# Kernel tuning notes

Hardware: AMD Instinct MI355X
Metric: run time of the kernel (lower is better)

Reference implementation:

```python
import jax, jax.numpy as jnp
import numpy as np

N_QUBITS = 10
N_LAYERS = 2

# ---- batched statevector simulator helpers (state shape: (B,) + (2,)*n) ----

def _apply1q(state, w, mat):
    # mat: [2,2] complex, same for all batch elements
    s = jnp.moveaxis(state, w + 1, 1)
    s = jnp.einsum('ij,bj...->bi...', mat, s)
    return jnp.moveaxis(s, 1, w + 1)

def _apply1q_b(state, w, mats):
    # mats: [B,2,2] complex, per-batch gate (input-encoding RY)
    s = jnp.moveaxis(state, w + 1, 1)
    s = jnp.einsum('bij,bj...->bi...', mats, s)
    return jnp.moveaxis(s, 1, w + 1)

def _cnot(state, c, t):
    s = jnp.moveaxis(state, (c + 1, t + 1), (1, 2))  # [B,2(ctrl),2(tgt),...]
    s = jnp.concatenate([s[:, :1], jnp.flip(s[:, 1:2], axis=2)], axis=1)
    return jnp.moveaxis(s, (1, 2), (c + 1, t + 1))

def _rz(t):
    p = jnp.exp(-0.5j * t.astype(jnp.complex64))
    z = jnp.zeros((), jnp.complex64)
    return jnp.stack([jnp.stack([p, z]), jnp.stack([z, jnp.conj(p)])])

def _rx(t):
    h = 0.5 * t
    c = jnp.cos(h).astype(jnp.complex64)
    s = jnp.sin(h).astype(jnp.complex64) * (-1j)
    return jnp.stack([jnp.stack([c, s]), jnp.stack([s, c])])

def _ry(t):
    h = 0.5 * t
    c, s = jnp.cos(h), jnp.sin(h)
    return jnp.stack([jnp.stack([c, -s]), jnp.stack([s, c])]).astype(jnp.complex64)

def qlayer(angles, qparams):
    """angles: [B, n_qubits] float -> [B, n_qubits] PauliZ expectations."""
    B = angles.shape[0]
    n = N_QUBITS
    state = jnp.zeros((B,) + (2,) * n, jnp.complex64)
    state = state.at[(slice(None),) + (0,) * n].set(1.0)
    # data-encoding RY with per-batch angles
    half = 0.5 * angles
    c, s = jnp.cos(half), jnp.sin(half)
    for w in range(n):
        row0 = jnp.stack([c[:, w], -s[:, w]], -1)
        row1 = jnp.stack([s[:, w], c[:, w]], -1)
        mats = jnp.stack([row0, row1], 1).astype(jnp.complex64)  # [B,2,2]
        state = _apply1q_b(state, w, mats)
    for l in range(N_LAYERS):
        for w in range(n):
            state = _apply1q(state, w, _rz(qparams[l, w, 0]))
            state = _apply1q(state, w, _rx(qparams[l, w, 1]))
            state = _apply1q(state, w, _ry(qparams[l, w, 2]))
        for w in range(n - 1):
            state = _cnot(state, w, w + 1)
        state = _cnot(state, n - 1, 0)
    probs = jnp.real(state * jnp.conj(state))
    exps = []
    for w in range(n):
        axes = tuple(a for a in range(1, n + 1) if a != w + 1)
        p = jnp.sum(probs, axis=axes)  # [B,2]
        exps.append(p[:, 0] - p[:, 1])
    return jnp.stack(exps, -1)


def setup_inputs() -> dict:
    key = jax.random.key(0)
    ks = jax.random.split(key, 12)
    T, B, D, H = 64, 256, 32, N_QUBITS
    in_dim = D + H
    std = 1.0 / np.sqrt(in_dim)
    inputs = jax.random.normal(ks[0], (T, B, D), jnp.float32)
    qparams = 0.01 * jax.random.normal(ks[1], (N_LAYERS, N_QUBITS, 3), jnp.float32)
    def lin(k1, k2):
        W = jax.random.uniform(k1, (H, in_dim), jnp.float32, -std, std)
        b = jax.random.uniform(k2, (H,), jnp.float32, -std, std)
        return W, b
    W_f, b_f = lin(ks[2], ks[3])
    W_i, b_i = lin(ks[4], ks[5])
    W_g, b_g = lin(ks[6], ks[7])
    W_o, b_o = lin(ks[8], ks[9])
    return dict(inputs=inputs, qparams=qparams, W_f=W_f, b_f=b_f, W_i=W_i, b_i=b_i,
                W_g=W_g, b_g=b_g, W_o=W_o, b_o=b_o)


def reference(inputs, qparams, W_f, b_f, W_i, b_i, W_g, b_g, W_o, b_o):
    T, B, D = inputs.shape
    H = N_QUBITS

    def step(carry, x):
        hx, cx = carry
        comb = jnp.concatenate([x, hx], axis=1)  # [B, D+H]
        pre = jnp.concatenate([
            comb @ W_f.T + b_f,
            comb @ W_i.T + b_i,
            comb @ W_g.T + b_g,
            comb @ W_o.T + b_o,
        ], axis=0)  # [4B, H] -- one fused circuit call for all 4 gates
        q = qlayer(pre, qparams).reshape(4, B, H)
        f = jax.nn.sigmoid(q[0])
        i = jax.nn.sigmoid(q[1])
        g = jnp.tanh(q[2])
        o = jax.nn.sigmoid(q[3])
        cx2 = f * cx + i * g
        hx2 = o * jnp.tanh(cx2)
        return (hx2, cx2), hx2

    hx = jnp.zeros((B, H), jnp.float32)
    cx = jnp.zeros((B, H), jnp.float32)
    (hx, cx), outputs = jax.lax.scan(jax.checkpoint(step), (hx, cx), inputs)
    return outputs, hx, cx
```

## Files before the change

kernel.cpp:

```cpp
#include <hip/hip_runtime.h>

#define TS 64
#define NB 256
#define DI 32
#define NH 10
#define IND 42

template<int CTRL>
__device__ __forceinline__ float dppx(float v){
  return __int_as_float(__builtin_amdgcn_update_dpp(
      0, __float_as_int(v), CTRL, 0xF, 0xF, true));
}

__device__ __forceinline__ float rl(float v, int lane){
  return __int_as_float(__builtin_amdgcn_readlane(__float_as_int(v), lane));
}

__device__ __forceinline__ void pin(float& x){ asm volatile("" : "+v"(x)); }

__device__ __forceinline__ float sigm(float x){ return 1.f/(1.f + __expf(-x)); }
__device__ __forceinline__ float tanhr(float x){ float e = __expf(2.f*x); return 1.f - 2.f/(e + 1.f); }

__device__ __forceinline__ void mkU(float t1, float t2, float t3, float* dst){
  float c1 = __cosf(0.5f*t1), s1 = __sinf(0.5f*t1);
  float c2 = __cosf(0.5f*t2), s2 = __sinf(0.5f*t2);
  float c3 = __cosf(0.5f*t3), s3 = __sinf(0.5f*t3);
  float A00r =  c2*c1, A00i = -c2*s1;
  float A01r =  s2*s1, A01i = -s2*c1;
  float A10r = -s2*s1, A10i = -s2*c1;
  float A11r =  c2*c1, A11i =  c2*s1;
  dst[0] = c3*A00r - s3*A10r; dst[1] = c3*A00i - s3*A10i;
  dst[2] = c3*A01r - s3*A11r; dst[3] = c3*A01i - s3*A11i;
  dst[4] = s3*A00r + c3*A10r; dst[5] = s3*A00i + c3*A10i;
  dst[6] = s3*A01r + c3*A11r; dst[7] = s3*A01i + c3*A11i;
}

__device__ __forceinline__ float3 qf(float q00, float q11, float q01){
  return make_float3(0.5f*(q00+q11), 0.5f*(q00-q11), 0.5f*q01);
}
__device__ __forceinline__ float qeval(float3 q, float C, float S){
  return fmaf(q.y, C, fmaf(q.z, S, q.x));
}

__global__ __launch_bounds__(256) __attribute__((amdgpu_waves_per_eu(1, 1)))
void qlstm_kernel(const float* __restrict__ xin,
                  const float* __restrict__ qp,
                  const float* __restrict__ Wf, const float* __restrict__ bfp,
                  const float* __restrict__ Wi, const float* __restrict__ bip,
                  const float* __restrict__ Wg, const float* __restrict__ bgp,
                  const float* __restrict__ Wo, const float* __restrict__ bop,
                  float* __restrict__ out)
{
  __shared__ float lx[TS][DI + 1];
  __shared__ float lwx[4][TS][NH];
  __shared__ __align__(16) float lBw[4][NH][4];
  __shared__ __align__(16) float lq[2][NH][4];

  const int tid  = threadIdx.x;
  const int b    = blockIdx.x;
  const int g    = tid >> 6;
  const int lane = tid & 63;
  const int hq   = lane >> 2;
  const int sg   = lane & 3;
  const int hrow = (lane < NH) ? lane : 0;

  const float* Wsel = (g==0) ? Wf : (g==1) ? Wi : (g==2) ? Wg : Wo;
  const float* bsel = (g==0) ? bfp : (g==1) ? bip : (g==2) ? bgp : bop;

  for (int i = tid; i < TS*DI; i += 256) {
    int tt = i >> 5, d = i & 31;
    lx[tt][d] = xin[(size_t)tt*(NB*DI) + b*DI + d];
  }
  if (lane < NH) {
    float u[8];
    mkU(qp[30 + lane*3 + 0], qp[30 + lane*3 + 1], qp[30 + lane*3 + 2], u);
    float B00 = u[0]*u[0]+u[1]*u[1] - (u[4]*u[4]+u[5]*u[5]);
    float B11 = u[2]*u[2]+u[3]*u[3] - (u[6]*u[6]+u[7]*u[7]);
    float B01r= u[0]*u[2]+u[1]*u[3] - (u[4]*u[6]+u[5]*u[7]);
    float B01i= u[1]*u[2]-u[0]*u[3] - (u[5]*u[6]-u[4]*u[7]);
    *reinterpret_cast<float4*>(&lBw[g][lane][0]) = make_float4(B00,B11,B01r,B01i);
  }
  __syncthreads();

  {
    float acc[NH];
    #pragma unroll
    for (int h = 0; h < NH; h++) acc[h] = bsel[h];
    for (int k = 0; k < DI; k++) {
      float xk = lx[lane][k];
      #pragma unroll
      for (int h = 0; h < NH; h++) acc[h] = fmaf(Wsel[h*IND + k], xk, acc[h]);
    }
    #pragma unroll
    for (int h = 0; h < NH; h++) lwx[g][lane][h] = acc[h];
  }

  float wh[NH];
  #pragma unroll
  for (int j = 0; j < NH; j++) wh[j] = Wsel[hrow*IND + DI + j];

  float3 Qn0, Qn1, Qer, Qei;
  {
    float U1[8];
    mkU(qp[hrow*3+0], qp[hrow*3+1], qp[hrow*3+2], U1);
    float r00r=U1[0], r00i=U1[1], r01r=U1[2], r01i=U1[3];
    float r10r=U1[4], r10i=U1[5], r11r=U1[6], r11i=U1[7];
    float P0r,P0i,P1r,P1i, R0r,R0i,R1r,R1i;
    if (lane == 0) {
      P0r=r00r; P0i=r00i; P1r=r01r; P1i=r01i;
      R0r=r10r; R0i=r10i; R1r=r11r; R1i=r11i;
    } else {
      P0r=0.5f*(r00r+r10r); P0i=0.5f*(r00i+r10i);
      P1r=0.5f*(r01r+r11r); P1i=0.5f*(r01i+r11i);
      R0r=0.5f*(r00r-r10r); R0i=0.5f*(r00i-r10i);
      R1r=0.5f*(r01r-r11r); R1i=0.5f*(r01i-r11i);
    }
    Qn0 = qf(P0r*P0r+P0i*P0i, P1r*P1r+P1i*P1i, 2.f*(P0r*P1r+P0i*P1i));
    Qn1 = qf(R0r*R0r+R0i*R0i, R1r*R1r+R1i*R1i, 2.f*(R0r*R1r+R0i*R1i));
    Qer = qf(R0r*P0r+R0i*P0i, R1r*P1r+R1i*P1i,
             (R0r*P1r+R0i*P1i) + (R1r*P0r+R1i*P0i));
    Qei = qf(R0i*P0r-R0r*P0i, R1i*P1r-R1r*P1i,
             (R0i*P1r-R0r*P1i) + (R1i*P0r-R1r*P0i));
  }

  float4 b0 = *reinterpret_cast<const float4*>(&lBw[g][0][0]);
  if (hq == 0) b0 = make_float4(1.f, 1.f, 0.f, 0.f);
  float k0, k3, ka, kb;
  if      (sg == 0) { k0 = b0.x;  k3 = b0.y;  ka = b0.z; kb = -b0.w; }
  else if (sg == 1) { k0 = b0.z;  k3 = b0.z;  ka = 0.5f*(b0.x + b0.y); kb = 0.f; }
  else if (sg == 2) { k0 = -b0.w; k3 = b0.w;  ka = 0.f;  kb = 0.5f*(b0.y - b0.x); }
  else              { k0 = b0.y;  k3 = b0.x;  ka = b0.z; kb = b0.w; }
  {
    const float pw = (sg == 1) ? 2.f : (sg == 2) ? -2.f : 1.f;
    k0 *= pw; k3 *= pw; ka *= pw; kb *= pw;
  }

  float C00[9], C11[9], Cr[9], Ci[9];
  #pragma unroll
  for (int w = 1; w <= 9; w++) {
    float4 bb = *reinterpret_cast<const float4*>(&lBw[g][w][0]);
    bool inM = (hq == 0) || (w <= hq);
    C00[w-1] = inM ? bb.x : 1.f;
    C11[w-1] = inM ? bb.y : 1.f;
    Cr[w-1]  = inM ? bb.z : 0.f;
    Ci[w-1]  = inM ? bb.w : 0.f;
  }

  #pragma unroll
  for (int w = 0; w < 9; w++) {
    pin(C00[w]); pin(C11[w]); pin(Cr[w]); pin(Ci[w]);
  }
  #pragma unroll
  for (int j = 0; j < NH; j++) pin(wh[j]);
  pin(Qn0.x); pin(Qn0.y); pin(Qn0.z);
  pin(Qn1.x); pin(Qn1.y); pin(Qn1.z);
  pin(Qer.x); pin(Qer.y); pin(Qer.z);
  pin(Qei.x); pin(Qei.y); pin(Qei.z);
  pin(k0); pin(k3); pin(ka); pin(kb);

  const float se = (g == 2) ? -2.f : -1.f;
  const float sa = (g == 2) ?  2.f :  1.f;
  const float sb = (g == 2) ? -1.f :  0.f;

  float cstate = 0.f, hval = 0.f;
  float wxcur = lwx[g][0][hrow];

  for (int t = 0; t < TS; t++) {
    const int tb = t & 1;

    float h0 = rl(hval,0), h1 = rl(hval,1), h2 = rl(hval,2), h3 = rl(hval,3), h4 = rl(hval,4);
    float h5 = rl(hval,5), h6 = rl(hval,6), h7 = rl(hval,7), h8 = rl(hval,8), h9 = rl(hval,9);
    float p0 = fmaf(wh[1], h1, wh[0]*h0);
    float p1 = fmaf(wh[3], h3, wh[2]*h2);
    float p2 = fmaf(wh[5], h5, wh[4]*h4);
    float p3 = fmaf(wh[7], h7, wh[6]*h6);
    float p4 = fmaf(wh[9], h9, wh[8]*h8);
    float pre = wxcur + ((p0 + p1) + (p2 + p3) + p4);

    wxcur = lwx[g][(t+1) & (TS-1)][hrow];

    float th = pre * 0.15915494309189535f;
    float S = __builtin_amdgcn_sinf(th);
    float C = __builtin_amdgcn_cosf(th);
    float n0v  = qeval(Qn0, C, S);
    float n1v  = qeval(Qn1, C, S);
    float e1rv = qeval(Qer, C, S);
    float e1iv = qeval(Qei, C, S);

    float vx0 = rl(n0v,0), vy0 = rl(n1v,0), vr0 = rl(e1rv,0), vi0 = rl(e1iv,0);
    float r0 = k0*vx0;
    float r3 = k3*vy0;
    float a  = ka*vr0 - kb*vi0;
    float bz = ka*vi0 + kb*vr0;
    #pragma unroll
    for (int w = 1; w <= 9; w++) {
      float vxw = rl(n0v, w), vyw = rl(n1v, w), vrw = rl(e1rv, w), viw = rl(e1iv, w);
      float q  = r0 + r3,  t2a = a + a;
      float u0 = q + t2a,  u3 = q - t2a;
      float s  = r0 - r3,  bb = bz + bz;
      float m0 = u0 * vxw;
      float m3 = u3 * vyw;
      float am = s*vrw + bb*viw;
      float bm = s*viw - bb*vrw;
      float q2 = m0 + m3,  t2m = am + am;
      float y0 = q2 + t2m, y3 = q2 - t2m;
      float s2 = m0 - m3,  b2 = bm + bm;
      r0 = y0 * C00[w-1];
      r3 = y3 * C11[w-1];
      a  = s2*Cr[w-1] - b2*Ci[w-1];
      bz = -(s2*Ci[w-1] + b2*Cr[w-1]);
    }

    float t0 = (sg & 1) ? a  : r0;
    float t1 = (sg & 1) ? r3 : bz;
    float Ee = (sg & 2) ? t1 : t0;
    Ee += dppx<0xB1>(Ee);
    Ee += dppx<0x4E>(Ee);
    if ((lane & 3) == 0 && hq < NH) {
      lq[tb][hq][g] = fmaf(sa, 1.f/(1.f + __expf(se*Ee)), sb);
    }
    __syncthreads();

    float4 gates = *reinterpret_cast<const float4*>(&lq[tb][hrow][0]);
    cstate = gates.x*cstate + gates.y*gates.z;
    hval = gates.w*tanhr(cstate);
    if (g == 0 && lane < NH) out[(size_t)t*(NB*NH) + b*NH + lane] = hval;
  }

  if (g == 0 && lane < NH) {
    out[(size_t)TS*NB*NH + b*NH + lane]          = hval;
    out[(size_t)TS*NB*NH + NB*NH + b*NH + lane]  = cstate;
  }
}

extern "C" void kernel_launch(void* const* d_in, const int* in_sizes, int n_in,
                              void* d_out, int out_size, void* d_ws, size_t ws_size,
                              hipStream_t stream) {
  (void)in_sizes; (void)n_in; (void)d_ws; (void)ws_size; (void)out_size;
  qlstm_kernel<<<dim3(NB), dim3(256), 0, stream>>>(
      (const float*)d_in[0], (const float*)d_in[1],
      (const float*)d_in[2], (const float*)d_in[3],
      (const float*)d_in[4], (const float*)d_in[5],
      (const float*)d_in[6], (const float*)d_in[7],
      (const float*)d_in[8], (const float*)d_in[9],
      (float*)d_out);
}
```

Measured before the change: 123.7 us.

## Pack two batch elements per block to run two waves per SIMD

Each block now processes two batch elements with 512 threads, halving the grid and setting waves_per_eu to 2. The aim is to hide the latency of the serial per-timestep chain by interleaving two independent waves on each SIMD. In exchange, only half the CUs are used, the register budget per wave shrinks, and the block-wide barrier now couples the two independent sequences.

```diff
diff --git a/kernel.cpp b/kernel.cpp
--- a/kernel.cpp
+++ b/kernel.cpp
@@ -42,7 +42,7 @@
   return fmaf(q.y, C, fmaf(q.z, S, q.x));
 }
 
-__global__ __launch_bounds__(256) __attribute__((amdgpu_waves_per_eu(1, 1)))
+__global__ __launch_bounds__(512) __attribute__((amdgpu_waves_per_eu(2, 2)))
 void qlstm_kernel(const float* __restrict__ xin,
                   const float* __restrict__ qp,
                   const float* __restrict__ Wf, const float* __restrict__ bfp,
@@ -51,14 +51,15 @@
                   const float* __restrict__ Wo, const float* __restrict__ bop,
                   float* __restrict__ out)
 {
-  __shared__ float lx[TS][DI + 1];
-  __shared__ float lwx[4][TS][NH];
-  __shared__ __align__(16) float lBw[4][NH][4];
-  __shared__ __align__(16) float lq[2][NH][4];
+  __shared__ float lx[2][TS][DI + 1];
+  __shared__ float lwx[2][4][TS][NH];
+  __shared__ __align__(16) float lBw[2][4][NH][4];
+  __shared__ __align__(16) float lq[2][2][NH][4];
 
   const int tid  = threadIdx.x;
-  const int b    = blockIdx.x;
-  const int g    = tid >> 6;
+  const int sub  = tid >> 8;
+  const int b    = blockIdx.x * 2 + sub;
+  const int g    = (tid >> 6) & 3;
   const int lane = tid & 63;
   const int hq   = lane >> 2;
   const int sg   = lane & 3;
@@ -67,9 +68,9 @@
   const float* Wsel = (g==0) ? Wf : (g==1) ? Wi : (g==2) ? Wg : Wo;
   const float* bsel = (g==0) ? bfp : (g==1) ? bip : (g==2) ? bgp : bop;
 
-  for (int i = tid; i < TS*DI; i += 256) {
-    int tt = i >> 5, d = i & 31;
-    lx[tt][d] = xin[(size_t)tt*(NB*DI) + b*DI + d];
+  for (int i = tid; i < 2*TS*DI; i += 512) {
+    int ss = i >> 11, r = i & 2047, tt = r >> 5, d = r & 31;
+    lx[ss][tt][d] = xin[(size_t)tt*(NB*DI) + (size_t)(blockIdx.x*2 + ss)*DI + d];
   }
   if (lane < NH) {
     float u[8];
@@ -78,7 +79,7 @@
     float B11 = u[2]*u[2]+u[3]*u[3] - (u[6]*u[6]+u[7]*u[7]);
     float B01r= u[0]*u[2]+u[1]*u[3] - (u[4]*u[6]+u[5]*u[7]);
     float B01i= u[1]*u[2]-u[0]*u[3] - (u[5]*u[6]-u[4]*u[7]);
-    *reinterpret_cast<float4*>(&lBw[g][lane][0]) = make_float4(B00,B11,B01r,B01i);
+    *reinterpret_cast<float4*>(&lBw[sub][g][lane][0]) = make_float4(B00,B11,B01r,B01i);
   }
   __syncthreads();
 
@@ -87,12 +88,12 @@
     #pragma unroll
     for (int h = 0; h < NH; h++) acc[h] = bsel[h];
     for (int k = 0; k < DI; k++) {
-      float xk = lx[lane][k];
+      float xk = lx[sub][lane][k];
       #pragma unroll
       for (int h = 0; h < NH; h++) acc[h] = fmaf(Wsel[h*IND + k], xk, acc[h]);
     }
     #pragma unroll
-    for (int h = 0; h < NH; h++) lwx[g][lane][h] = acc[h];
+    for (int h = 0; h < NH; h++) lwx[sub][g][lane][h] = acc[h];
   }
 
   float wh[NH];
@@ -123,7 +124,7 @@
              (R0i*P1r-R0r*P1i) + (R1i*P0r-R1r*P0i));
   }
 
-  float4 b0 = *reinterpret_cast<const float4*>(&lBw[g][0][0]);
+  float4 b0 = *reinterpret_cast<const float4*>(&lBw[sub][g][0][0]);
   if (hq == 0) b0 = make_float4(1.f, 1.f, 0.f, 0.f);
   float k0, k3, ka, kb;
   if      (sg == 0) { k0 = b0.x;  k3 = b0.y;  ka = b0.z; kb = -b0.w; }
@@ -138,7 +139,7 @@
   float C00[9], C11[9], Cr[9], Ci[9];
   #pragma unroll
   for (int w = 1; w <= 9; w++) {
-    float4 bb = *reinterpret_cast<const float4*>(&lBw[g][w][0]);
+    float4 bb = *reinterpret_cast<const float4*>(&lBw[sub][g][w][0]);
     bool inM = (hq == 0) || (w <= hq);
     C00[w-1] = inM ? bb.x : 1.f;
     C11[w-1] = inM ? bb.y : 1.f;
@@ -163,7 +164,7 @@
   const float sb = (g == 2) ? -1.f :  0.f;
 
   float cstate = 0.f, hval = 0.f;
-  float wxcur = lwx[g][0][hrow];
+  float wxcur = lwx[sub][g][0][hrow];
 
   for (int t = 0; t < TS; t++) {
     const int tb = t & 1;
@@ -177,7 +178,7 @@
     float p4 = fmaf(wh[9], h9, wh[8]*h8);
     float pre = wxcur + ((p0 + p1) + (p2 + p3) + p4);
 
-    wxcur = lwx[g][(t+1) & (TS-1)][hrow];
+    wxcur = lwx[sub][g][(t+1) & (TS-1)][hrow];
 
     float th = pre * 0.15915494309189535f;
     float S = __builtin_amdgcn_sinf(th);
@@ -217,11 +218,11 @@
     Ee += dppx<0xB1>(Ee);
     Ee += dppx<0x4E>(Ee);
     if ((lane & 3) == 0 && hq < NH) {
-      lq[tb][hq][g] = fmaf(sa, 1.f/(1.f + __expf(se*Ee)), sb);
+      lq[sub][tb][hq][g] = fmaf(sa, 1.f/(1.f + __expf(se*Ee)), sb);
     }
     __syncthreads();
 
-    float4 gates = *reinterpret_cast<const float4*>(&lq[tb][hrow][0]);
+    float4 gates = *reinterpret_cast<const float4*>(&lq[sub][tb][hrow][0]);
     cstate = gates.x*cstate + gates.y*gates.z;
     hval = gates.w*tanhr(cstate);
     if (g == 0 && lane < NH) out[(size_t)t*(NB*NH) + b*NH + lane] = hval;
@@ -237,7 +238,7 @@
                               void* d_out, int out_size, void* d_ws, size_t ws_size,
                               hipStream_t stream) {
   (void)in_sizes; (void)n_in; (void)d_ws; (void)ws_size; (void)out_size;
-  qlstm_kernel<<<dim3(NB), dim3(256), 0, stream>>>(
+  qlstm_kernel<<<dim3(NB/2), dim3(512), 0, stream>>>(
       (const float*)d_in[0], (const float*)d_in[1],
       (const float*)d_in[2], (const float*)d_in[3],
       (const float*)d_in[4], (const float*)d_in[5],
```

Result: slower. 151.1 us (+22.1%).
